# Kernel optimization log

Measured on AMD Instinct MI355X. Metric: run time of the kernel, lower is better.

The kernel has to match this reference:

```python
import jax, jax.numpy as jnp
import numpy as np

B, S, D, H, T = 512, 256, 64, 256, 50
IN = 2 * D + 1  # LSTM input dim = input_size*2+1
NSUB = 8       # RK4 substeps per output interval
TIME_OFFSET = 0.0

def _xavier(k, shape):
    fan_out, fan_in = shape
    lim = float(np.sqrt(6.0 / (fan_in + fan_out)))
    return jax.random.uniform(k, shape, minval=-lim, maxval=lim, dtype=jnp.float32)

def setup_inputs() -> dict:
    key = jax.random.key(0)
    ks = jax.random.split(key, 12)
    gaps = jax.random.uniform(ks[3], (B, T), minval=0.05, maxval=0.2, dtype=jnp.float32)
    return {
        "x": jax.random.normal(ks[0], (B, S, IN), jnp.float32),
        "lengths": jax.random.randint(ks[1], (B,), S // 2, S + 1),
        "label_feature": jax.random.normal(ks[2], (B, T, D), jnp.float32),
        "label_time": jnp.cumsum(gaps, axis=1),  # sorted per-sample times
        "label_mask": (jax.random.uniform(ks[4], (B, T, D)) < 0.2).astype(jnp.float32),
        "W_ih": _xavier(ks[5], (4 * H, IN)),
        "W_hh": _xavier(ks[6], (4 * H, H)),
        "b_ih": jnp.zeros((4 * H,), jnp.float32),
        "b_hh": jnp.zeros((4 * H,), jnp.float32),
        "Wp1": _xavier(ks[7], (H, H)), "bp1": jnp.zeros((H,), jnp.float32),
        "Wp2": _xavier(ks[8], (D, H)), "bp2": jnp.zeros((D,), jnp.float32),
        "Wd1": _xavier(ks[9], (H, D)), "bd1": jnp.zeros((H,), jnp.float32),
        "Wd2": _xavier(ks[10], (D, H)), "bd2": jnp.zeros((D,), jnp.float32),
    }

def _forward(x, label_feature, label_time, label_mask,
             W_ih, W_hh, b_ih, b_hh, Wp1, bp1, Wp2, bp2, Wd1, bd1, Wd2, bd2,
             lengths):
    # --- LSTM encoder (PyTorch gate order i, f, g, o) ---
    xW = jnp.einsum('bsi,gi->bsg', x, W_ih) + b_ih  # [B,S,4H]
    h0 = jnp.zeros((x.shape[0], H), x.dtype)
    def step(carry, xt):
        h, c = carry
        g = xt + h @ W_hh.T + b_hh
        i, f, gg, o = jnp.split(g, 4, axis=-1)
        c = jax.nn.sigmoid(f) * c + jax.nn.sigmoid(i) * jnp.tanh(gg)
        h = jax.nn.sigmoid(o) * jnp.tanh(c)
        return (h, c), h
    _, hs = jax.lax.scan(step, (h0, h0), jnp.swapaxes(xW, 0, 1))
    hs = jnp.swapaxes(hs, 0, 1)  # [B,S,H]
    # masked mean over valid timesteps
    mask = (jnp.arange(x.shape[1])[None, :] < lengths[:, None]).astype(x.dtype)
    pooled = (hs * mask[:, :, None]).sum(axis=1) / lengths[:, None].astype(x.dtype)
    # projection MLP -> initial ODE state
    y0 = jax.nn.relu(pooled @ Wp1.T + bp1) @ Wp2.T + bp2  # [B,D]
    # --- batched Neural-ODE integration (fixed-step RK4) ---
    def deriv(y):
        return jax.nn.relu(y @ Wd1.T + bd1) @ Wd2.T + bd2
    ts = label_time - TIME_OFFSET
    dts = (ts[:, 1:] - ts[:, :-1]) / NSUB  # [B,T-1]
    def interval(y, dt_b):
        dt = dt_b[:, None]
        for _ in range(NSUB):
            k1 = deriv(y)
            k2 = deriv(y + 0.5 * dt * k1)
            k3 = deriv(y + 0.5 * dt * k2)
            k4 = deriv(y + dt * k3)
            y = y + (dt / 6.0) * (k1 + 2.0 * k2 + 2.0 * k3 + k4)
        return y, y
    _, traj = jax.lax.scan(interval, y0, jnp.swapaxes(dts, 0, 1))  # [T-1,B,D]
    predict = jnp.swapaxes(jnp.concatenate([y0[None], traj], axis=0), 0, 1)  # [B,T,D]
    loss = (predict - label_feature) ** 2 * (1.0 - label_mask)
    return predict, loss

def reference(x, lengths, label_feature, label_time, label_mask,
              W_ih, W_hh, b_ih, b_hh, Wp1, bp1, Wp2, bp2, Wd1, bd1, Wd2, bd2):
    return _forward(x, label_feature, label_time, label_mask,
                    W_ih, W_hh, b_ih, b_hh, Wp1, bp1, Wp2, bp2, Wd1, bd1, Wd2, bd2,
                    lengths)
```

## Files before the change

### kernel.cpp

```cpp
#include <hip/hip_runtime.h>
#include <hip/hip_bf16.h>

#define BB 512
#define SS 256
#define HH 256
#define DD 64
#define TT 50
#define GG 1024
#define INW 129

typedef _Float16 h4 __attribute__((ext_vector_type(4)));
typedef _Float16 h8 __attribute__((ext_vector_type(8)));
typedef __fp16 hf2 __attribute__((ext_vector_type(2)));
typedef float f32x4 __attribute__((ext_vector_type(4)));
typedef unsigned int u32;

__device__ inline float sigf(float x) { return 1.f / (1.f + __expf(-x)); }
__device__ inline float tanhf_(float x) { return 1.f - 2.f / (__expf(2.f * x) + 1.f); }

__device__ inline u32 pkrtz(float a, float b) {
    hf2 h = __builtin_amdgcn_cvt_pkrtz(a, b);
    return __builtin_bit_cast(u32, h);
}

__global__ __launch_bounds__(256) void prep_kernel(
    const float* __restrict__ W_hh, const float* __restrict__ W_ih,
    const float* __restrict__ Wd1, const float* __restrict__ Wd2,
    h4* __restrict__ BhhV4, h4* __restrict__ BhhL4, h4* __restrict__ BhhS4,
    _Float16* __restrict__ Bih, h4* __restrict__ A1f4, h4* __restrict__ A2f4)
{
    int idx = blockIdx.x * 256 + threadIdx.x;
    if (idx < 65536) {
        int eh = idx & 1;
        int l = (idx >> 1) & 63;
        int ks = (idx >> 7) & 7;
        int s = (idx >> 10) & 7;
        int w = (idx >> 13) & 7;
        int g = s & 3, jt = s >> 2;
        int n = g * 256 + w * 32 + jt * 16 + (l & 15);
        int k = 32 * ks + 8 * (l >> 4) + 4 * eh;
        float4 v = *(const float4*)(W_hh + (size_t)n * HH + k);
        h4 o; o[0] = (_Float16)v.x; o[1] = (_Float16)v.y; o[2] = (_Float16)v.z; o[3] = (_Float16)v.w;
        if (ks < 4)      BhhV4[(((w * 8 + s) * 4 + ks) * 64 + l) * 2 + eh] = o;
        else if (ks < 6) BhhL4[(((w * 8 + s) * 2 + (ks - 4)) * 64 + l) * 2 + eh] = o;
        else             BhhS4[(((w * 8 + s) * 2 + (ks - 6)) * 64 + l) * 2 + eh] = o;
    } else if (idx < 106496) {
        int fj = idx - 65536;
        int eh = fj & 1;
        int l = (fj >> 1) & 63;
        int si = fj >> 7;
        int ks = si % 5;
        int ntile = si / 5;
        int n = ntile * 16 + (l & 15);
        int k = 32 * ks + 8 * (l >> 4) + 4 * eh;
        h4 o;
#pragma unroll
        for (int i = 0; i < 4; i++) {
            int kk = k + i;
            o[i] = (_Float16)((kk < INW) ? W_ih[(size_t)n * INW + kk] : 0.f);
        }
        *(h4*)(Bih + (size_t)fj * 4) = o;
    } else if (idx < 110592) {
        int fj = idx - 106496;
        int eh = fj & 1;
        int l = (fj >> 1) & 63;
        int slot = fj >> 7;
        int ks = slot & 1, t = slot >> 1;
        int row = 16 * t + (l & 15);
        int k = 32 * ks + 8 * (l >> 4) + 4 * eh;
        h4 o;
#pragma unroll
        for (int i = 0; i < 4; i++) o[i] = (_Float16)Wd1[(size_t)row * DD + k + i];
        A1f4[fj] = o;
    } else if (idx < 114688) {
        int fj = idx - 110592;
        int eh = fj & 1;
        int l = (fj >> 1) & 63;
        int slot = fj >> 7;
        int ks = slot & 7, t2 = slot >> 3;
        int row = 16 * t2 + (l & 15);
        int k = 32 * ks + 8 * (l >> 4) + 4 * eh;
        h4 o;
#pragma unroll
        for (int i = 0; i < 4; i++) o[i] = (_Float16)Wd2[(size_t)row * HH + k + i];
        A2f4[fj] = o;
    }
}

__global__ __launch_bounds__(256) void xw_kernel(
    const float* __restrict__ x, const _Float16* __restrict__ Bih,
    const float* __restrict__ b_ih, const float* __restrict__ b_hh,
    h4* __restrict__ xwf)
{
    __shared__ __align__(16) _Float16 ash[4][5][64][8];
    int tid = threadIdx.x;
    int w4 = tid >> 6, l = tid & 63;
    int bx = blockIdx.x;
    int t = bx >> 3, Bb = bx & 7;

    for (int i = tid; i < 64 * 160; i += 256) {
        int rr = i / 160, kk = i % 160;
        float v = (kk < INW) ? x[((size_t)(Bb * 64 + rr) * SS + t) * INW + kk] : 0.f;
        ash[rr >> 4][kk >> 5][(((kk & 31) >> 3) << 4) + (rr & 15)][kk & 7] = (_Float16)v;
    }
    __syncthreads();

    h8 A[4][5];
#pragma unroll
    for (int ms = 0; ms < 4; ms++)
#pragma unroll
        for (int ks = 0; ks < 5; ks++)
            A[ms][ks] = *(h8*)&ash[ms][ks][l][0];

    const h8* Bih8 = (const h8*)Bih;
    for (int nt16 = 0; nt16 < 16; nt16++) {
        int ntile = w4 * 16 + nt16;
        h8 Bv[5];
#pragma unroll
        for (int ks = 0; ks < 5; ks++) Bv[ks] = Bih8[(ntile * 5 + ks) * 64 + l];
        int nb = ntile * 16 + (l & 15);
        float bias = b_ih[nb] + b_hh[nb];
        f32x4 acc[4];
#pragma unroll
        for (int ms = 0; ms < 4; ms++) acc[ms] = (f32x4){0.f, 0.f, 0.f, 0.f};
#pragma unroll
        for (int ks = 0; ks < 5; ks++)
#pragma unroll
            for (int ms = 0; ms < 4; ms++)
                acc[ms] = __builtin_amdgcn_mfma_f32_16x16x32_f16(A[ms][ks], Bv[ks], acc[ms], 0, 0, 0);
        int slot = ((ntile & 15) >> 1) * 8 + (ntile & 1) * 4 + (ntile >> 4);
#pragma unroll
        for (int ms = 0; ms < 4; ms++) {
            int bg = Bb * 4 + ms;
            h4 o;
#pragma unroll
            for (int r = 0; r < 4; r++) o[r] = (_Float16)(acc[ms][r] + bias);
            xwf[(((size_t)bg * SS + t) * 64 + slot) * 64 + l] = o;
        }
    }
}

__global__ __launch_bounds__(512, 2) void lstm_kernel(
    const h8* __restrict__ BhhV, const h8* __restrict__ BhhL, const h8* __restrict__ BhhS,
    const h4* __restrict__ xwf, const int* __restrict__ lengths, float* __restrict__ pooled)
{
    __shared__ __align__(16) _Float16 Wlds[65536];
    __shared__ __align__(16) _Float16 hst[2][4096];
    int tid = threadIdx.x;
    int w = tid >> 6, l = tid & 63;
    int q = l >> 4, b0 = l & 15;
    int bg = blockIdx.x;

    {
        const uint4* src = (const uint4*)BhhL;
        uint4* dst = (uint4*)Wlds;
#pragma unroll
        for (int i = 0; i < 16; i++) dst[i * 512 + tid] = src[i * 512 + tid];
    }

    h8 Wv[8][4];
#pragma unroll
    for (int s = 0; s < 8; s++)
#pragma unroll
        for (int ks = 0; ks < 4; ks++)
            Wv[s][ks] = BhhV[((w * 8 + s) * 4 + ks) * 64 + l];

    int len_[4];
    float c_[2][4], pa[2][4];
#pragma unroll
    for (int r = 0; r < 4; r++) {
        len_[r] = lengths[bg * 16 + 4 * q + r];
#pragma unroll
        for (int jt = 0; jt < 2; jt++) { c_[jt][r] = 0.f; pa[jt][r] = 0.f; }
    }

    {
        uint4* hz = (uint4*)hst;
        hz[tid] = make_uint4(0, 0, 0, 0);
        hz[512 + tid] = make_uint4(0, 0, 0, 0);
    }
    __syncthreads();

    h4 xc[8], xn[8];
    {
        const h4* p0 = xwf + (((size_t)bg * SS + 0) * 64 + w * 8) * 64 + l;
#pragma unroll
        for (int s = 0; s < 8; s++) xc[s] = p0[s * 64];
    }

    int cur = 0;
    for (int t = 0; t < SS; t++) {
        int tn = (t + 1) & 255;
        const h4* pn = xwf + (((size_t)bg * SS + tn) * 64 + w * 8) * 64 + l;
#pragma unroll
        for (int s = 0; s < 8; s++) xn[s] = pn[s * 64];

        int zoff = 0;
        asm volatile("" : "+v"(zoff));
        const h8* bS = BhhS + zoff;
#pragma unroll
        for (int jt = 0; jt < 2; jt++) {
            h8 Ws[8];
#pragma unroll
            for (int g = 0; g < 4; g++) {
                Ws[g]     = bS[((w * 8 + jt * 4 + g) * 2 + 0) * 64 + l];
                Ws[4 + g] = bS[((w * 8 + jt * 4 + g) * 2 + 1) * 64 + l];
            }
            f32x4 acc[4];
#pragma unroll
            for (int g = 0; g < 4; g++) acc[g] = (f32x4){0.f, 0.f, 0.f, 0.f};
#pragma unroll
            for (int ks = 0; ks < 4; ks++) {
                h8 A = *(const h8*)&hst[cur][(b0 * 256 + 32 * ks + 8 * q) ^ ((b0 & 7) << 3)];
#pragma unroll
                for (int g = 0; g < 4; g++)
                    acc[g] = __builtin_amdgcn_mfma_f32_16x16x32_f16(A, Wv[jt * 4 + g][ks], acc[g], 0, 0, 0);
            }
#pragma unroll
            for (int ks = 4; ks < 6; ks++) {
                h8 A = *(const h8*)&hst[cur][(b0 * 256 + 32 * ks + 8 * q) ^ ((b0 & 7) << 3)];
#pragma unroll
                for (int g = 0; g < 4; g++) {
                    h8 Bw = *(const h8*)&Wlds[(((w * 8 + jt * 4 + g) * 2 + (ks - 4)) * 64 + l) * 8];
                    acc[g] = __builtin_amdgcn_mfma_f32_16x16x32_f16(A, Bw, acc[g], 0, 0, 0);
                }
            }
            {
                h8 A = *(const h8*)&hst[cur][(b0 * 256 + 32 * 6 + 8 * q) ^ ((b0 & 7) << 3)];
#pragma unroll
                for (int g = 0; g < 4; g++)
                    acc[g] = __builtin_amdgcn_mfma_f32_16x16x32_f16(A, Ws[g], acc[g], 0, 0, 0);
            }
            {
                h8 A = *(const h8*)&hst[cur][(b0 * 256 + 32 * 7 + 8 * q) ^ ((b0 & 7) << 3)];
#pragma unroll
                for (int g = 0; g < 4; g++)
                    acc[g] = __builtin_amdgcn_mfma_f32_16x16x32_f16(A, Ws[4 + g], acc[g], 0, 0, 0);
            }
#pragma unroll
            for (int r = 0; r < 4; r++) {
                float gi = acc[0][r] + (float)xc[jt * 4 + 0][r];
                float gf = acc[1][r] + (float)xc[jt * 4 + 1][r];
                float gg = acc[2][r] + (float)xc[jt * 4 + 2][r];
                float go = acc[3][r] + (float)xc[jt * 4 + 3][r];
                float cc = sigf(gf) * c_[jt][r] + sigf(gi) * tanhf_(gg);
                c_[jt][r] = cc;
                float hh = sigf(go) * tanhf_(cc);
                if (t < len_[r]) pa[jt][r] += hh;
                int b = 4 * q + r;
                int j = w * 32 + jt * 16 + b0;
                hst[cur ^ 1][(b * 256 + j) ^ ((b & 7) << 3)] = (_Float16)hh;
            }
        }
        __syncthreads();
#pragma unroll
        for (int s = 0; s < 8; s++) xc[s] = xn[s];
        cur ^= 1;
    }

#pragma unroll
    for (int jt = 0; jt < 2; jt++)
#pragma unroll
        for (int r = 0; r < 4; r++) {
            int b = 4 * q + r;
            int j = w * 32 + jt * 16 + b0;
            pooled[(size_t)(bg * 16 + b) * HH + j] = pa[jt][r] / (float)len_[r];
        }
}

__global__ __launch_bounds__(256) void head_kernel(
    const float* __restrict__ pooled, const float* __restrict__ Wp1,
    const float* __restrict__ bp1, const float* __restrict__ Wp2,
    const float* __restrict__ bp2, float* __restrict__ y0ws)
{
    __shared__ __align__(16) float psh[HH];
    __shared__ __align__(16) float rsh[HH];
    int tid = threadIdx.x, b = blockIdx.x;
    psh[tid] = pooled[(size_t)b * HH + tid];
    __syncthreads();
    float a = bp1[tid];
    const float* wr = Wp1 + (size_t)tid * HH;
#pragma unroll 8
    for (int k = 0; k < HH; k += 4) {
        float4 w = *(const float4*)(wr + k);
        a += psh[k] * w.x + psh[k + 1] * w.y + psh[k + 2] * w.z + psh[k + 3] * w.w;
    }
    rsh[tid] = fmaxf(a, 0.f);
    __syncthreads();
    if (tid < DD) {
        float acc = bp2[tid];
        const float* w2 = Wp2 + (size_t)tid * HH;
#pragma unroll 8
        for (int h = 0; h < HH; h += 4) {
            float4 w = *(const float4*)(w2 + h);
            acc += rsh[h] * w.x + rsh[h + 1] * w.y + rsh[h + 2] * w.z + rsh[h + 3] * w.w;
        }
        y0ws[(size_t)b * DD + tid] = acc;
    }
}

__global__ __launch_bounds__(256) void ode_kernel(
    const float* __restrict__ y0ws, const h8* __restrict__ A1f,
    const float* __restrict__ bd1, const h8* __restrict__ A2f,
    const float* __restrict__ bd2, const float* __restrict__ ltime,
    const float* __restrict__ lfeat, const float* __restrict__ lmask,
    float* __restrict__ pred, float* __restrict__ losso)
{
    __shared__ __align__(16) _Float16 hX[4096];
    __shared__ __align__(16) _Float16 kX[1024];
    int tid = threadIdx.x;
    int wv = tid >> 6, l = tid & 63;
    int q = l >> 4, bb = l & 15;
    int b = blockIdx.x * 16 + bb;

    h8 A1[4][2];
#pragma unroll
    for (int tt = 0; tt < 4; tt++)
#pragma unroll
        for (int ks = 0; ks < 2; ks++)
            A1[tt][ks] = A1f[((4 * wv + tt) * 2 + ks) * 64 + l];
    h8 A2[8];
#pragma unroll
    for (int ks = 0; ks < 8; ks++) A2[ks] = A2f[(wv * 8 + ks) * 64 + l];

    float bd1c[4][4];
#pragma unroll
    for (int tt = 0; tt < 4; tt++)
#pragma unroll
        for (int r = 0; r < 4; r++) bd1c[tt][r] = bd1[16 * (4 * wv + tt) + 4 * q + r];
    float bd2c[4];
#pragma unroll
    for (int r = 0; r < 4; r++) bd2c[r] = bd2[16 * wv + 4 * q + r];

    float y[16], kp[16], ksum[16];
#pragma unroll
    for (int ks = 0; ks < 2; ks++)
#pragma unroll
        for (int e = 0; e < 8; e++) {
            y[ks * 8 + e] = y0ws[(size_t)b * DD + 32 * ks + 8 * q + e];
            kp[ks * 8 + e] = 0.f;
        }

    if (wv == 0) {
#pragma unroll
        for (int ks = 0; ks < 2; ks++) {
            size_t idx = ((size_t)b * TT + 0) * DD + 32 * ks + 8 * q;
            float4 p0 = make_float4(y[ks * 8 + 0], y[ks * 8 + 1], y[ks * 8 + 2], y[ks * 8 + 3]);
            float4 p1 = make_float4(y[ks * 8 + 4], y[ks * 8 + 5], y[ks * 8 + 6], y[ks * 8 + 7]);
            *(float4*)&pred[idx] = p0;
            *(float4*)&pred[idx + 4] = p1;
            float4 lf0 = *(const float4*)&lfeat[idx], lf1 = *(const float4*)&lfeat[idx + 4];
            float4 lm0 = *(const float4*)&lmask[idx], lm1 = *(const float4*)&lmask[idx + 4];
            float4 lo0, lo1;
            lo0.x = (p0.x - lf0.x) * (p0.x - lf0.x) * (1.f - lm0.x);
            lo0.y = (p0.y - lf0.y) * (p0.y - lf0.y) * (1.f - lm0.y);
            lo0.z = (p0.z - lf0.z) * (p0.z - lf0.z) * (1.f - lm0.z);
            lo0.w = (p0.w - lf0.w) * (p0.w - lf0.w) * (1.f - lm0.w);
            lo1.x = (p1.x - lf1.x) * (p1.x - lf1.x) * (1.f - lm1.x);
            lo1.y = (p1.y - lf1.y) * (p1.y - lf1.y) * (1.f - lm1.y);
            lo1.z = (p1.z - lf1.z) * (p1.z - lf1.z) * (1.f - lm1.z);
            lo1.w = (p1.w - lf1.w) * (p1.w - lf1.w) * (1.f - lm1.w);
            *(float4*)&losso[idx] = lo0;
            *(float4*)&losso[idx + 4] = lo1;
        }
    }

    for (int iv = 0; iv < TT - 1; iv++) {
        float t0 = ltime[(size_t)b * TT + iv], t1 = ltime[(size_t)b * TT + iv + 1];
        float dt = (t1 - t0) * 0.125f;
        for (int ss = 0; ss < 8; ss++) {
#pragma unroll
            for (int i = 0; i < 16; i++) ksum[i] = 0.f;
            const float AE[4] = {0.f, 0.5f, 0.5f, 1.f};
            const float WE[4] = {1.f, 2.f, 2.f, 1.f};
#pragma unroll
            for (int e = 0; e < 4; e++) {
                h8 B1[2];
#pragma unroll
                for (int ks = 0; ks < 2; ks++) {
                    float ye[8];
#pragma unroll
                    for (int i = 0; i < 8; i++) ye[i] = y[ks * 8 + i] + AE[e] * dt * kp[ks * 8 + i];
                    uint4 u;
                    u.x = pkrtz(ye[0], ye[1]); u.y = pkrtz(ye[2], ye[3]);
                    u.z = pkrtz(ye[4], ye[5]); u.w = pkrtz(ye[6], ye[7]);
                    B1[ks] = __builtin_bit_cast(h8, u);
                }
                f32x4 C1[4];
#pragma unroll
                for (int tt = 0; tt < 4; tt++) C1[tt] = (f32x4){0.f, 0.f, 0.f, 0.f};
#pragma unroll
                for (int ks = 0; ks < 2; ks++)
#pragma unroll
                    for (int tt = 0; tt < 4; tt++)
                        C1[tt] = __builtin_amdgcn_mfma_f32_16x16x32_f16(A1[tt][ks], B1[ks], C1[tt], 0, 0, 0);
#pragma unroll
                for (int tt = 0; tt < 4; tt++) {
                    float h0 = fmaxf(C1[tt][0] + bd1c[tt][0], 0.f);
                    float h1 = fmaxf(C1[tt][1] + bd1c[tt][1], 0.f);
                    float h2 = fmaxf(C1[tt][2] + bd1c[tt][2], 0.f);
                    float h3 = fmaxf(C1[tt][3] + bd1c[tt][3], 0.f);
                    int i0 = 16 * (4 * wv + tt) + 4 * q;
                    int idx = (bb * 256 + i0) ^ ((bb & 7) << 3);
                    *(uint2*)&hX[idx] = make_uint2(pkrtz(h0, h1), pkrtz(h2, h3));
                }
                __syncthreads();
                f32x4 Ca = (f32x4){0.f, 0.f, 0.f, 0.f}, Cb = (f32x4){0.f, 0.f, 0.f, 0.f};
#pragma unroll
                for (int ks = 0; ks < 8; ks += 2) {
                    h8 B2a = *(const h8*)&hX[(bb * 256 + 32 * ks + 8 * q) ^ ((bb & 7) << 3)];
                    h8 B2b = *(const h8*)&hX[(bb * 256 + 32 * (ks + 1) + 8 * q) ^ ((bb & 7) << 3)];
                    Ca = __builtin_amdgcn_mfma_f32_16x16x32_f16(A2[ks], B2a, Ca, 0, 0, 0);
                    Cb = __builtin_amdgcn_mfma_f32_16x16x32_f16(A2[ks + 1], B2b, Cb, 0, 0, 0);
                }
                {
                    float k0 = Ca[0] + Cb[0] + bd2c[0];
                    float k1 = Ca[1] + Cb[1] + bd2c[1];
                    float k2 = Ca[2] + Cb[2] + bd2c[2];
                    float k3 = Ca[3] + Cb[3] + bd2c[3];
                    int j0 = 16 * wv + 4 * q;
                    int idx = (bb * 64 + j0) ^ ((bb & 7) << 3);
                    *(uint2*)&kX[idx] = make_uint2(pkrtz(k0, k1), pkrtz(k2, k3));
                }
                __syncthreads();
#pragma unroll
                for (int ks = 0; ks < 2; ks++) {
                    h8 kvh = *(const h8*)&kX[(bb * 64 + 32 * ks + 8 * q) ^ ((bb & 7) << 3)];
#pragma unroll
                    for (int i = 0; i < 8; i++) {
                        float kvf = (float)kvh[i];
                        kp[ks * 8 + i] = kvf;
                        ksum[ks * 8 + i] += WE[e] * kvf;
                    }
                }
            }
#pragma unroll
            for (int i = 0; i < 16; i++) y[i] += dt * (1.f / 6.f) * ksum[i];
        }
        if (wv == 0) {
#pragma unroll
            for (int ks = 0; ks < 2; ks++) {
                size_t idx = ((size_t)b * TT + iv + 1) * DD + 32 * ks + 8 * q;
                float4 p0 = make_float4(y[ks * 8 + 0], y[ks * 8 + 1], y[ks * 8 + 2], y[ks * 8 + 3]);
                float4 p1 = make_float4(y[ks * 8 + 4], y[ks * 8 + 5], y[ks * 8 + 6], y[ks * 8 + 7]);
                *(float4*)&pred[idx] = p0;
                *(float4*)&pred[idx + 4] = p1;
                float4 lf0 = *(const float4*)&lfeat[idx], lf1 = *(const float4*)&lfeat[idx + 4];
                float4 lm0 = *(const float4*)&lmask[idx], lm1 = *(const float4*)&lmask[idx + 4];
                float4 lo0, lo1;
                lo0.x = (p0.x - lf0.x) * (p0.x - lf0.x) * (1.f - lm0.x);
                lo0.y = (p0.y - lf0.y) * (p0.y - lf0.y) * (1.f - lm0.y);
                lo0.z = (p0.z - lf0.z) * (p0.z - lf0.z) * (1.f - lm0.z);
                lo0.w = (p0.w - lf0.w) * (p0.w - lf0.w) * (1.f - lm0.w);
                lo1.x = (p1.x - lf1.x) * (p1.x - lf1.x) * (1.f - lm1.x);
                lo1.y = (p1.y - lf1.y) * (p1.y - lf1.y) * (1.f - lm1.y);
                lo1.z = (p1.z - lf1.z) * (p1.z - lf1.z) * (1.f - lm1.z);
                lo1.w = (p1.w - lf1.w) * (p1.w - lf1.w) * (1.f - lm1.w);
                *(float4*)&losso[idx] = lo0;
                *(float4*)&losso[idx + 4] = lo1;
            }
        }
    }
}

extern "C" void kernel_launch(void* const* d_in, const int* in_sizes, int n_in,
                              void* d_out, int out_size, void* d_ws, size_t ws_size,
                              hipStream_t stream)
{
    const float* x      = (const float*)d_in[0];
    const int* lengths  = (const int*)d_in[1];
    const float* lfeat  = (const float*)d_in[2];
    const float* ltime  = (const float*)d_in[3];
    const float* lmask  = (const float*)d_in[4];
    const float* W_ih   = (const float*)d_in[5];
    const float* W_hh   = (const float*)d_in[6];
    const float* b_ih   = (const float*)d_in[7];
    const float* b_hh   = (const float*)d_in[8];
    const float* Wp1    = (const float*)d_in[9];
    const float* bp1    = (const float*)d_in[10];
    const float* Wp2    = (const float*)d_in[11];
    const float* bp2    = (const float*)d_in[12];
    const float* Wd1    = (const float*)d_in[13];
    const float* bd1    = (const float*)d_in[14];
    const float* Wd2    = (const float*)d_in[15];
    const float* bd2    = (const float*)d_in[16];

    float* pred  = (float*)d_out;
    float* losso = pred + (size_t)BB * TT * DD;

    char* ws = (char*)d_ws;
    h4*       xwf    = (h4*)(ws + 0);
    h4*       BhhV   = (h4*)(ws + 268435456);
    h4*       BhhL   = (h4*)(ws + 268697600);
    h4*       BhhS   = (h4*)(ws + 268828672);
    _Float16* Bih    = (_Float16*)(ws + 268959744);
    float*    pooled = (float*)(ws + 269287424);
    float*    y0ws   = (float*)(ws + 269811712);
    h4*       A1f    = (h4*)(ws + 269942784);
    h4*       A2f    = (h4*)(ws + 269975552);

    prep_kernel<<<448, 256, 0, stream>>>(W_hh, W_ih, Wd1, Wd2, BhhV, BhhL, BhhS, Bih, A1f, A2f);
    xw_kernel<<<2048, 256, 0, stream>>>(x, Bih, b_ih, b_hh, xwf);
    lstm_kernel<<<32, 512, 0, stream>>>((const h8*)BhhV, (const h8*)BhhL, (const h8*)BhhS,
                                        xwf, lengths, pooled);
    head_kernel<<<BB, 256, 0, stream>>>(pooled, Wp1, bp1, Wp2, bp2, y0ws);
    ode_kernel<<<32, 256, 0, stream>>>(y0ws, (const h8*)A1f, bd1, (const h8*)A2f, bd2,
                                       ltime, lfeat, lmask, pred, losso);
}
```

Baseline: 2.673 ms.

## Relayout LSTM hidden buffer, drop x prefetch, run ODE one sample per block

The LSTM hidden-state LDS buffer becomes an MFMA-fragment-ordered layout, so A operands are read as contiguous per-lane h8 loads with no XOR swizzle. The xW register prefetch for the next timestep is replaced by direct per-jt loads, and the BhhS weight loads are split into two halves to cut register pressure. The ODE kernel launches 512 blocks, each integrating a single sample with all 16 MFMA rows computing the same sample, in exchange for 16x redundant math. The aim is more parallelism in the ODE stage, but only row 0 writes outputs and the hidden-state writes in the new layout may cause LDS bank conflicts.

New measurement: 2.561 ms. 1.04x faster.

```diff
diff --git a/kernel.cpp b/kernel.cpp
--- a/kernel.cpp
+++ b/kernel.cpp
@@ -145,10 +145,9 @@
     const h4* __restrict__ xwf, const int* __restrict__ lengths, float* __restrict__ pooled)
 {
     __shared__ __align__(16) _Float16 Wlds[65536];
-    __shared__ __align__(16) _Float16 hst[2][4096];
+    __shared__ __align__(16) _Float16 hbuf[2][8][64][8];
     int tid = threadIdx.x;
     int w = tid >> 6, l = tid & 63;
-    int q = l >> 4, b0 = l & 15;
     int bg = blockIdx.x;
 
     {
@@ -169,56 +168,54 @@
     float c_[2][4], pa[2][4];
 #pragma unroll
     for (int r = 0; r < 4; r++) {
-        len_[r] = lengths[bg * 16 + 4 * q + r];
+        int b = 4 * (l >> 4) + r;
+        len_[r] = lengths[bg * 16 + b];
 #pragma unroll
         for (int jt = 0; jt < 2; jt++) { c_[jt][r] = 0.f; pa[jt][r] = 0.f; }
     }
 
     {
-        uint4* hz = (uint4*)hst;
+        uint4* hz = (uint4*)hbuf;
         hz[tid] = make_uint4(0, 0, 0, 0);
         hz[512 + tid] = make_uint4(0, 0, 0, 0);
     }
     __syncthreads();
 
-    h4 xc[8], xn[8];
-    {
-        const h4* p0 = xwf + (((size_t)bg * SS + 0) * 64 + w * 8) * 64 + l;
-#pragma unroll
-        for (int s = 0; s < 8; s++) xc[s] = p0[s * 64];
-    }
-
     int cur = 0;
     for (int t = 0; t < SS; t++) {
-        int tn = (t + 1) & 255;
-        const h4* pn = xwf + (((size_t)bg * SS + tn) * 64 + w * 8) * 64 + l;
-#pragma unroll
-        for (int s = 0; s < 8; s++) xn[s] = pn[s * 64];
-
+        const h4* xpb = xwf + (((size_t)bg * SS + t) * 64 + w * 8) * 64 + l;
         int zoff = 0;
         asm volatile("" : "+v"(zoff));
         const h8* bS = BhhS + zoff;
 #pragma unroll
         for (int jt = 0; jt < 2; jt++) {
-            h8 Ws[8];
-#pragma unroll
-            for (int g = 0; g < 4; g++) {
-                Ws[g]     = bS[((w * 8 + jt * 4 + g) * 2 + 0) * 64 + l];
-                Ws[4 + g] = bS[((w * 8 + jt * 4 + g) * 2 + 1) * 64 + l];
-            }
+            h4 xv[4];
+#pragma unroll
+            for (int g = 0; g < 4; g++) xv[g] = xpb[(jt * 4 + g) * 64];
+            h8 Ws[4];
+#pragma unroll
+            for (int g = 0; g < 4; g++) Ws[g] = bS[((w * 8 + jt * 4 + g) * 2 + 0) * 64 + l];
             f32x4 acc[4];
 #pragma unroll
             for (int g = 0; g < 4; g++) acc[g] = (f32x4){0.f, 0.f, 0.f, 0.f};
 #pragma unroll
             for (int ks = 0; ks < 4; ks++) {
-                h8 A = *(const h8*)&hst[cur][(b0 * 256 + 32 * ks + 8 * q) ^ ((b0 & 7) << 3)];
+                h8 A = *(const h8*)&hbuf[cur][ks][l][0];
 #pragma unroll
                 for (int g = 0; g < 4; g++)
                     acc[g] = __builtin_amdgcn_mfma_f32_16x16x32_f16(A, Wv[jt * 4 + g][ks], acc[g], 0, 0, 0);
             }
+            {
+                h8 A = *(const h8*)&hbuf[cur][6][l][0];
+#pragma unroll
+                for (int g = 0; g < 4; g++)
+                    acc[g] = __builtin_amdgcn_mfma_f32_16x16x32_f16(A, Ws[g], acc[g], 0, 0, 0);
+            }
+#pragma unroll
+            for (int g = 0; g < 4; g++) Ws[g] = bS[((w * 8 + jt * 4 + g) * 2 + 1) * 64 + l];
 #pragma unroll
             for (int ks = 4; ks < 6; ks++) {
-                h8 A = *(const h8*)&hst[cur][(b0 * 256 + 32 * ks + 8 * q) ^ ((b0 & 7) << 3)];
+                h8 A = *(const h8*)&hbuf[cur][ks][l][0];
 #pragma unroll
                 for (int g = 0; g < 4; g++) {
                     h8 Bw = *(const h8*)&Wlds[(((w * 8 + jt * 4 + g) * 2 + (ks - 4)) * 64 + l) * 8];
@@ -226,35 +223,27 @@
                 }
             }
             {
-                h8 A = *(const h8*)&hst[cur][(b0 * 256 + 32 * 6 + 8 * q) ^ ((b0 & 7) << 3)];
+                h8 A = *(const h8*)&hbuf[cur][7][l][0];
 #pragma unroll
                 for (int g = 0; g < 4; g++)
                     acc[g] = __builtin_amdgcn_mfma_f32_16x16x32_f16(A, Ws[g], acc[g], 0, 0, 0);
             }
-            {
-                h8 A = *(const h8*)&hst[cur][(b0 * 256 + 32 * 7 + 8 * q) ^ ((b0 & 7) << 3)];
-#pragma unroll
-                for (int g = 0; g < 4; g++)
-                    acc[g] = __builtin_amdgcn_mfma_f32_16x16x32_f16(A, Ws[4 + g], acc[g], 0, 0, 0);
-            }
 #pragma unroll
             for (int r = 0; r < 4; r++) {
-                float gi = acc[0][r] + (float)xc[jt * 4 + 0][r];
-                float gf = acc[1][r] + (float)xc[jt * 4 + 1][r];
-                float gg = acc[2][r] + (float)xc[jt * 4 + 2][r];
-                float go = acc[3][r] + (float)xc[jt * 4 + 3][r];
+                float gi = acc[0][r] + (float)xv[0][r];
+                float gf = acc[1][r] + (float)xv[1][r];
+                float gg = acc[2][r] + (float)xv[2][r];
+                float go = acc[3][r] + (float)xv[3][r];
                 float cc = sigf(gf) * c_[jt][r] + sigf(gi) * tanhf_(gg);
                 c_[jt][r] = cc;
                 float hh = sigf(go) * tanhf_(cc);
                 if (t < len_[r]) pa[jt][r] += hh;
-                int b = 4 * q + r;
-                int j = w * 32 + jt * 16 + b0;
-                hst[cur ^ 1][(b * 256 + j) ^ ((b & 7) << 3)] = (_Float16)hh;
+                int b = 4 * (l >> 4) + r;
+                int j = w * 32 + jt * 16 + (l & 15);
+                hbuf[cur ^ 1][j >> 5][(((j & 31) >> 3) << 4) + b][j & 7] = (_Float16)hh;
             }
         }
         __syncthreads();
-#pragma unroll
-        for (int s = 0; s < 8; s++) xc[s] = xn[s];
         cur ^= 1;
     }
 
@@ -262,8 +251,8 @@
     for (int jt = 0; jt < 2; jt++)
 #pragma unroll
         for (int r = 0; r < 4; r++) {
-            int b = 4 * q + r;
-            int j = w * 32 + jt * 16 + b0;
+            int b = 4 * (l >> 4) + r;
+            int j = w * 32 + jt * 16 + (l & 15);
             pooled[(size_t)(bg * 16 + b) * HH + j] = pa[jt][r] / (float)len_[r];
         }
 }
@@ -311,7 +300,7 @@
     int tid = threadIdx.x;
     int wv = tid >> 6, l = tid & 63;
     int q = l >> 4, bb = l & 15;
-    int b = blockIdx.x * 16 + bb;
+    int b = blockIdx.x;
 
     h8 A1[4][2];
 #pragma unroll
@@ -341,7 +330,7 @@
             kp[ks * 8 + e] = 0.f;
         }
 
-    if (wv == 0) {
+    if (wv == 0 && bb == 0) {
 #pragma unroll
         for (int ks = 0; ks < 2; ks++) {
             size_t idx = ((size_t)b * TT + 0) * DD + 32 * ks + 8 * q;
@@ -437,7 +426,7 @@
 #pragma unroll
             for (int i = 0; i < 16; i++) y[i] += dt * (1.f / 6.f) * ksum[i];
         }
-        if (wv == 0) {
+        if (wv == 0 && bb == 0) {
 #pragma unroll
             for (int ks = 0; ks < 2; ks++) {
                 size_t idx = ((size_t)b * TT + iv + 1) * DD + 32 * ks + 8 * q;
@@ -504,6 +493,6 @@
     lstm_kernel<<<32, 512, 0, stream>>>((const h8*)BhhV, (const h8*)BhhL, (const h8*)BhhS,
                                         xwf, lengths, pooled);
     head_kernel<<<BB, 256, 0, stream>>>(pooled, Wp1, bp1, Wp2, bp2, y0ws);
-    ode_kernel<<<32, 256, 0, stream>>>(y0ws, (const h8*)A1f, bd1, (const h8*)A2f, bd2,
-                                       ltime, lfeat, lmask, pred, losso);
-}
+    ode_kernel<<<512, 256, 0, stream>>>(y0ws, (const h8*)A1f, bd1, (const h8*)A2f, bd2,
+                                        ltime, lfeat, lmask, pred, losso);
+}
```
